# Performance work log

Measured on AMD Instinct MI355X. Metric: run time of the kernel, lower is better.

Reference implementation:

```python
import jax, jax.numpy as jnp
import numpy as np

B, N, F, H, OUT, K, L = 32, 2048, 3, 64, 128, 16, 3


def _edge_mlp(e, w1, b1, wo, bo):
    # Faithful to the given MLP.forward: layer1 -> ReLU -> output (layer2 is skipped!)
    return jax.nn.relu(e @ w1 + b1) @ wo + bo


def _dynamic_edge_conv(x, k, w1, b1, wo, bo):
    # x: [B, N, D]. kNN in feature space (self included, distance 0), per graph.
    sq = jnp.sum(x * x, axis=-1)                                   # [B, N]
    d2 = sq[:, :, None] + sq[:, None, :] - 2.0 * jnp.einsum('bnd,bmd->bnm', x, x)
    _, idx = jax.lax.top_k(-d2, k)                                 # [B, N, K]
    x_j = jax.vmap(lambda xb, ib: xb[ib])(x, idx)                  # [B, N, K, D] gather
    x_i = jnp.broadcast_to(x[:, :, None, :], x_j.shape)
    e = jnp.concatenate([x_i, x_j - x_i], axis=-1)                 # EdgeConv message [B,N,K,2D]
    h = _edge_mlp(e, w1, b1, wo, bo)                               # [B, N, K, H]
    return jnp.mean(h, axis=2)                                     # aggr='mean' -> [B, N, H]


def setup_inputs() -> dict:
    key = jax.random.key(0)
    ks = jax.random.split(key, 20)
    inp = {'x': jax.random.normal(ks[0], (B, N, F), dtype=jnp.float32)}
    kit = iter(ks[1:])
    for i in range(L):
        din = 2 * F if i == 0 else 2 * H
        inp[f'w1_{i}'] = jax.random.normal(next(kit), (din, H), jnp.float32) / np.sqrt(din)
        inp[f'b1_{i}'] = jnp.zeros((H,), jnp.float32)
        inp[f'wo_{i}'] = jax.random.normal(next(kit), (H, H), jnp.float32) / np.sqrt(H)
        inp[f'bo_{i}'] = jnp.zeros((H,), jnp.float32)
    inp['fw1'] = jax.random.normal(next(kit), (H, H), jnp.float32) / np.sqrt(H)
    inp['fb1'] = jnp.zeros((H,), jnp.float32)
    inp['fw2'] = jax.random.normal(next(kit), (H, OUT), jnp.float32) / np.sqrt(H)
    inp['fb2'] = jnp.zeros((OUT,), jnp.float32)
    return inp


def reference(x, w1_0, b1_0, wo_0, bo_0, w1_1, b1_1, wo_1, bo_1, w1_2, b1_2, wo_2, bo_2, fw1, fb1, fw2, fb2):
    layers = [(w1_0, b1_0, wo_0, bo_0), (w1_1, b1_1, wo_1, bo_1), (w1_2, b1_2, wo_2, bo_2)]
    h = x
    for (w1, b1, wo, bo) in layers:
        h = _dynamic_edge_conv(h, K, w1, b1, wo, bo)
    g = jnp.mean(h, axis=1)                                        # global_mean_pool -> [B, H]
    return jax.nn.relu(g @ fw1 + fb1) @ fw2 + fb2                  # [B, OUT]
```

## Files before the change

### kernel.cpp

```cpp
#include <hip/hip_runtime.h>

#define BB 32
#define NN 2048
#define FF 3
#define HH 64
#define OUTC 128
#define KK 16
#define BN (BB * NN)

typedef __attribute__((ext_vector_type(8))) __bf16 bf16x8;
typedef __attribute__((ext_vector_type(4))) float f32x4;

__device__ __forceinline__ unsigned int packkey(float d2, unsigned int m) {
    unsigned int bb = __builtin_bit_cast(unsigned int, d2);
    unsigned int msk = (unsigned int)((int)bb >> 31);
    unsigned int srt = bb ^ (msk | 0x80000000u);
    return (srt & 0xFFFFF800u) | m;
}

__device__ __forceinline__ void ce(unsigned int& a, unsigned int& b) {
    unsigned int lo = a < b ? a : b;
    unsigned int hi = a < b ? b : a;
    a = lo; b = hi;
}

__device__ __forceinline__ void sort16(unsigned int k[16]) {
#pragma unroll
    for (int p = 1; p < 16; p <<= 1)
#pragma unroll
        for (int q = p; q >= 1; q >>= 1)
#pragma unroll
            for (int j = q % p; j + q < 16; j += 2 * q)
#pragma unroll
                for (int i = 0; i < q; ++i) {
                    int x = i + j, y = i + j + q;
                    if (y < 16 && (x / (2 * p) == y / (2 * p))) ce(k[x], k[y]);
                }
}

__device__ __forceinline__ void merge16(unsigned int keys[16], const unsigned int nk[16]) {
    unsigned int t[16];
#pragma unroll
    for (int i = 0; i < 16; ++i) {
        unsigned int b = nk[15 - i];
        t[i] = keys[i] < b ? keys[i] : b;
    }
#pragma unroll
    for (int d = 8; d >= 1; d >>= 1)
#pragma unroll
        for (int i = 0; i < 16; ++i)
            if ((i & d) == 0) ce(t[i], t[i ^ d]);
#pragma unroll
    for (int i = 0; i < 16; ++i) keys[i] = t[i];
}

__global__ __launch_bounds__(256) void prep3_kernel(const float* __restrict__ x,
                                                    const float* __restrict__ w1,
                                                    const float* __restrict__ b1,
                                                    float* __restrict__ sqo,
                                                    float* __restrict__ P,
                                                    float* __restrict__ Q) {
    const int tid = threadIdx.x;
    const int h = tid & 63;
    const int pl = tid >> 6;
    const long p = (long)blockIdx.x * 4 + pl;
    const float* fp = x + p * 3;
    const float f0 = fp[0], f1 = fp[1], f2 = fp[2];
    if (h == 0) sqo[p] = f0 * f0 + f1 * f1 + f2 * f2;
    float accp = 0.f, accq = 0.f;
    const float fv[3] = {f0, f1, f2};
#pragma unroll
    for (int d = 0; d < 3; ++d) {
        float wa = w1[d * HH + h];
        float wb = w1[(3 + d) * HH + h];
        accp = fmaf(fv[d], wa - wb, accp);
        accq = fmaf(fv[d], wb, accq);
    }
    P[p * HH + h] = accp + b1[h];
    Q[p * HH + h] = accq;
}

__global__ __launch_bounds__(256) void prep64_kernel(const float* __restrict__ feat,
                                                     const float* __restrict__ w1,
                                                     const float* __restrict__ b1,
                                                     __bf16* __restrict__ fbf,
                                                     float* __restrict__ sqo,
                                                     float* __restrict__ P,
                                                     float* __restrict__ Q) {
    __shared__ float rows[64 * HH];
    const int tid = threadIdx.x;
    const int h = tid & 63;
    const int wv = tid >> 6;
    const long row0 = (long)blockIdx.x * 64;

    float wdiff[64], wbv[64];
#pragma unroll
    for (int d = 0; d < 64; ++d) {
        float wa = w1[d * HH + h];
        float wb_ = w1[(HH + d) * HH + h];
        wdiff[d] = wa - wb_;
        wbv[d] = wb_;
    }
    const float bv = b1[h];

    {
        const float4* src = (const float4*)(feat + row0 * HH);
        float4* dst = (float4*)rows;
#pragma unroll
        for (int i = 0; i < 4; ++i) dst[tid + 256 * i] = src[tid + 256 * i];
    }
    __syncthreads();

    for (int r = wv * 16; r < wv * 16 + 16; ++r) {
        const long p = row0 + r;
        float fvh = rows[r * HH + h];
        fbf[p * HH + h] = (__bf16)fvh;
        float s = fvh * fvh;
        s += __shfl_xor(s, 1);
        s += __shfl_xor(s, 2);
        s += __shfl_xor(s, 4);
        s += __shfl_xor(s, 8);
        s += __shfl_xor(s, 16);
        s += __shfl_xor(s, 32);
        if (h == 0) sqo[p] = s;

        float ap0 = 0.f, ap1 = 0.f, aq0 = 0.f, aq1 = 0.f;
#pragma unroll
        for (int d4 = 0; d4 < 16; ++d4) {
            float4 fv = *(const float4*)&rows[r * HH + d4 * 4];
            ap0 = fmaf(fv.x, wdiff[4 * d4 + 0], ap0);
            aq0 = fmaf(fv.x, wbv[4 * d4 + 0], aq0);
            ap1 = fmaf(fv.y, wdiff[4 * d4 + 1], ap1);
            aq1 = fmaf(fv.y, wbv[4 * d4 + 1], aq1);
            ap0 = fmaf(fv.z, wdiff[4 * d4 + 2], ap0);
            aq0 = fmaf(fv.z, wbv[4 * d4 + 2], aq0);
            ap1 = fmaf(fv.w, wdiff[4 * d4 + 3], ap1);
            aq1 = fmaf(fv.w, wbv[4 * d4 + 3], aq1);
        }
        P[p * HH + h] = (ap0 + ap1) + bv;
        Q[p * HH + h] = aq0 + aq1;
    }
}

__global__ __launch_bounds__(256) void knn3_filter_kernel(const float* __restrict__ x,
                                                          const float* __restrict__ sq,
                                                          unsigned short* __restrict__ idx32) {
    __shared__ float4 lds_c[256];
    __shared__ unsigned int Km[64 * 68];
    const int tid = threadIdx.x;
    const int xcd = blockIdx.x & 7;
    const int ii = blockIdx.x >> 3;
    const int b = xcd + 8 * (ii >> 5);
    const int rg = ii & 31;
    const long pbase = (long)b * NN;
    const int r = tid >> 2, slot = tid & 3;
    const int row = rg * 64 + r;

    const float* rp = x + (pbase + row) * 3;
    const float xr0 = rp[0], xr1 = rp[1], xr2 = rp[2];

    unsigned int keys[KK];
#pragma unroll
    for (int j = 0; j < KK; ++j) keys[j] = 0xFFFFFFFFu;

    float c0, c1, c2, c3;
    {
        const float* cp = x + (pbase + tid) * 3;
        c0 = cp[0]; c1 = cp[1]; c2 = cp[2]; c3 = sq[pbase + tid];
    }

    for (int t = 0; t < NN / 256; ++t) {
        __syncthreads();
        lds_c[tid] = make_float4(c0, c1, c2, c3);
        __syncthreads();
        if (t < NN / 256 - 1) {
            const int m = (t + 1) * 256 + tid;
            const float* cp = x + (pbase + m) * 3;
            c0 = cp[0]; c1 = cp[1]; c2 = cp[2]; c3 = sq[pbase + m];
        }
        const int cbase = slot * 64;
#pragma unroll
        for (int bb = 0; bb < 4; ++bb) {
            unsigned int nk[16];
#pragma unroll
            for (int cc = 0; cc < 16; ++cc) {
                float4 v = lds_c[cbase + bb * 16 + cc];
                float dot = fmaf(xr0, v.x, fmaf(xr1, v.y, xr2 * v.z));
                float d2 = fmaf(-2.0f, dot, v.w);
                nk[cc] = packkey(d2, (unsigned int)(t * 256 + cbase + bb * 16 + cc));
            }
            sort16(nk);
            merge16(keys, nk);
        }
    }

    {
        uint4* kw = (uint4*)&Km[r * 68 + slot * 16];
#pragma unroll
        for (int q = 0; q < 4; ++q)
            kw[q] = make_uint4(keys[4 * q], keys[4 * q + 1], keys[4 * q + 2], keys[4 * q + 3]);
    }
    __syncthreads();
    if (slot < 2) {
        const unsigned int* k0 = &Km[r * 68 + slot * 32];
        const unsigned int* k1 = k0 + 16;
        unsigned short ms[16];
#pragma unroll
        for (int j = 0; j < 16; ++j) {
            unsigned int a = k0[j], bv = k1[15 - j];
            ms[j] = (unsigned short)((a < bv ? a : bv) & 0x7FFu);
        }
        uint4* op = (uint4*)(idx32 + ((pbase + row) * 32 + slot * 16));
        op[0] = ((const uint4*)ms)[0];
        op[1] = ((const uint4*)ms)[1];
    }
}

#define APAD 80
#define DPAD 68

__global__ __launch_bounds__(256) void knn_filter_kernel(const __bf16* __restrict__ fbf,
                                                         const float* __restrict__ sq,
                                                         unsigned short* __restrict__ idx32) {
    __shared__ __align__(16) __bf16 Ab[64 * APAD];
    __shared__ __align__(16) __bf16 Bb[64 * APAD];
    __shared__ __align__(16) unsigned int Dt[64 * DPAD];
    __shared__ float SqC[64];

    const int tid = threadIdx.x;
    const int xcd = blockIdx.x & 7;
    const int ii = blockIdx.x >> 3;
    const int b = xcd + 8 * (ii >> 5);
    const int rg = ii & 31;
    const long pbase = (long)b * NN;
    const int row0 = rg * 64;
    const int ci = tid >> 2, ch = tid & 3;

    {
        const __bf16* src = fbf + (pbase + row0 + ci) * 64 + ch * 16;
        uint4 v0 = *(const uint4*)src;
        uint4 v1 = *(const uint4*)(src + 8);
        *(uint4*)&Ab[ci * APAD + ch * 16] = v0;
        *(uint4*)&Ab[ci * APAD + ch * 16 + 8] = v1;
    }
    __syncthreads();

    const int wv = tid >> 6, ln = tid & 63;
    const int n16 = ln & 15, quad = ln >> 4;
    bf16x8 af0, af1;
    {
        const __bf16* ap = &Ab[(wv * 16 + n16) * APAD + quad * 8];
        af0 = *(const bf16x8*)ap;
        af1 = *(const bf16x8*)(ap + 32);
    }

    const int r = tid >> 2, slot = tid & 3;
    unsigned int keys[KK];
#pragma unroll
    for (int j = 0; j < KK; ++j) keys[j] = 0xFFFFFFFFu;

    uint4 pv0, pv1;
    float psq;
    {
        const __bf16* src = fbf + (pbase + ci) * 64 + ch * 16;
        pv0 = *(const uint4*)src;
        pv1 = *(const uint4*)(src + 8);
        psq = (tid < 64) ? sq[pbase + tid] : 0.f;
    }

    for (int t = 0; t < NN / 64; ++t) {
        *(uint4*)&Bb[ci * APAD + ch * 16] = pv0;
        *(uint4*)&Bb[ci * APAD + ch * 16 + 8] = pv1;
        if (tid < 64) SqC[tid] = psq;
        __syncthreads();

#pragma unroll
        for (int ct = 0; ct < 4; ++ct) {
            const __bf16* bp = &Bb[(ct * 16 + n16) * APAD + quad * 8];
            bf16x8 bf0 = *(const bf16x8*)bp;
            bf16x8 bf1 = *(const bf16x8*)(bp + 32);
            f32x4 acc = {0.f, 0.f, 0.f, 0.f};
            acc = __builtin_amdgcn_mfma_f32_16x16x32_bf16(af0, bf0, acc, 0, 0, 0);
            acc = __builtin_amdgcn_mfma_f32_16x16x32_bf16(af1, bf1, acc, 0, 0, 0);
            const int ccol = ct * 16 + n16;
            const float sqc = SqC[ccol];
            const unsigned int m = (unsigned int)(t * 64 + ccol);
#pragma unroll
            for (int rr = 0; rr < 4; ++rr) {
                const int rrow = wv * 16 + quad * 4 + rr;
                Dt[rrow * DPAD + ccol] = packkey(fmaf(-2.0f, acc[rr], sqc), m);
            }
        }
        __syncthreads();

        if (t < NN / 64 - 1) {
            const __bf16* src = fbf + (pbase + (long)(t + 1) * 64 + ci) * 64 + ch * 16;
            pv0 = *(const uint4*)src;
            pv1 = *(const uint4*)(src + 8);
            if (tid < 64) psq = sq[pbase + (t + 1) * 64 + tid];
        }

        {
            const uint4* kp = (const uint4*)&Dt[r * DPAD + slot * 16];
            unsigned int nk[16];
#pragma unroll
            for (int q = 0; q < 4; ++q) {
                uint4 kv = kp[q];
                nk[4 * q + 0] = kv.x; nk[4 * q + 1] = kv.y;
                nk[4 * q + 2] = kv.z; nk[4 * q + 3] = kv.w;
            }
            sort16(nk);
            merge16(keys, nk);
        }
    }

    __syncthreads();
    {
        uint4* kw = (uint4*)&Dt[r * DPAD + slot * 16];
#pragma unroll
        for (int q = 0; q < 4; ++q)
            kw[q] = make_uint4(keys[4 * q], keys[4 * q + 1], keys[4 * q + 2], keys[4 * q + 3]);
    }
    __syncthreads();
    if (slot < 2) {
        const unsigned int* k0 = &Dt[r * DPAD + slot * 32];
        const unsigned int* k1 = k0 + 16;
        unsigned short ms[16];
#pragma unroll
        for (int j = 0; j < 16; ++j) {
            unsigned int a = k0[j], bv = k1[15 - j];
            ms[j] = (unsigned short)((a < bv ? a : bv) & 0x7FFu);
        }
        uint4* op = (uint4*)(idx32 + ((pbase + row0 + r) * 32 + slot * 16));
        op[0] = ((const uint4*)ms)[0];
        op[1] = ((const uint4*)ms)[1];
    }
}

template <int D>
__global__ __launch_bounds__(256) void rescore_gather_kernel(const float* __restrict__ feat,
                                                             const float* __restrict__ sq,
                                                             const unsigned short* __restrict__ idx32,
                                                             const float* __restrict__ P,
                                                             const float* __restrict__ Q,
                                                             const float* __restrict__ wo,
                                                             const float* __restrict__ bo,
                                                             float* __restrict__ outf) {
    __shared__ float rowf[8][D];
    __shared__ float Sc[8][32];
    __shared__ int Ji[8][32];
    __shared__ float Sq32[8][32];
    __shared__ int Li[8][KK];
    __shared__ float Rl[8][HH];
    const int tid = threadIdx.x;
    const int w = tid >> 6, ln = tid & 63;
    const int rw = ln >> 5, c = ln & 31;
    const int xcd = blockIdx.x & 7;
    const int ii = blockIdx.x >> 3;
    const int batch = xcd + 8 * (ii >> 8);
    const int rb = ii & 255;
    const long pbase = (long)batch * NN;
    const long pblk = pbase + (long)rb * 8;
    const long p = pblk + w * 2 + rw;
    const int row_ = w * 2 + rw;

    for (int i = tid; i < 8 * D; i += 256) rowf[i / D][i % D] = feat[pblk * D + i];
    {
        const int j0 = (int)idx32[p * 32 + c];
        Ji[row_][c] = j0;
        Sq32[row_][c] = sq[pbase + j0];
    }
    __syncthreads();

    if constexpr (D == 64) {
        const int cg = ln >> 2, e = ln & 3;
#pragma unroll
        for (int rr = 0; rr < 2; ++rr) {
#pragma unroll
            for (int pp = 0; pp < 2; ++pp) {
                const int row = w * 2 + rr;
                const int cand = pp * 16 + cg;
                const int jj = Ji[row][cand];
                const float* cb = feat + (pbase + jj) * 64;
                float part = 0.f;
#pragma unroll
                for (int blk = 0; blk < 4; ++blk) {
                    float4 cv = *(const float4*)(cb + blk * 16 + e * 4);
                    float4 rv = *(const float4*)&rowf[row][blk * 16 + e * 4];
                    part = fmaf(rv.x, cv.x, part);
                    part = fmaf(rv.y, cv.y, part);
                    part = fmaf(rv.z, cv.z, part);
                    part = fmaf(rv.w, cv.w, part);
                }
                part += __shfl_xor(part, 1);
                part += __shfl_xor(part, 2);
                if (e == 0) Sc[row][cand] = fmaf(-2.0f, part, Sq32[row][cand]);
            }
        }
    } else {
        const int jj = Ji[row_][c];
        const float* cp = feat + (pbase + jj) * 3;
        float dot = fmaf(rowf[row_][0], cp[0],
                    fmaf(rowf[row_][1], cp[1], rowf[row_][2] * cp[2]));
        Sc[row_][c] = fmaf(-2.0f, dot, Sq32[row_][c]);
    }
    __syncthreads();

    {
        const float score = Sc[row_][c];
        const int j = Ji[row_][c];
        int rank = 0;
#pragma unroll
        for (int m = 0; m < 32; ++m) {
            float dm = Sc[row_][m];
            int jm = Ji[row_][m];
            rank += (dm < score || (dm == score && jm < j)) ? 1 : 0;
        }
        if (rank < KK) Li[row_][rank] = j;
    }
    __syncthreads();

    const int h = tid & 63, pl = tid >> 6;
#pragma unroll
    for (int rr0 = 0; rr0 < 2; ++rr0) {
        const int rr = pl + rr0 * 4;
        const long pp = pblk + rr;
        const float Pv = P[pp * HH + h];
        float acc = 0.f;
#pragma unroll
        for (int k = 0; k < KK; ++k) {
            int j2 = Li[rr][k];
            acc += fmaxf(Pv + Q[(pbase + j2) * HH + h], 0.f);
        }
        Rl[rr][h] = acc * (1.f / KK);
    }
    __syncthreads();
#pragma unroll
    for (int rr0 = 0; rr0 < 2; ++rr0) {
        const int rr = pl + rr0 * 4;
        float o = bo[h];
#pragma unroll
        for (int l = 0; l < HH; ++l) o = fmaf(Rl[rr][l], wo[l * HH + h], o);
        outf[(pblk + rr) * HH + h] = o;
    }
}

__global__ __launch_bounds__(256) void pool_partial_kernel(const float* __restrict__ feat,
                                                           float* __restrict__ pp) {
    __shared__ float part[4][HH];
    const int batch = blockIdx.x >> 3;
    const int chk = blockIdx.x & 7;
    const int tid = threadIdx.x;
    const int h = tid & 63;
    const int sub = tid >> 6;
    float s = 0.f;
    const float* fp = feat + ((long)batch * NN + chk * 256 + sub * 64) * HH + h;
    for (int n = 0; n < 64; ++n) s += fp[(long)n * HH];
    part[sub][h] = s;
    __syncthreads();
    if (tid < HH)
        pp[(batch * 8 + chk) * HH + h] = part[0][h] + part[1][h] + part[2][h] + part[3][h];
}

__global__ __launch_bounds__(256) void head_kernel(const float* __restrict__ pp,
                                                   const float* __restrict__ fw1,
                                                   const float* __restrict__ fb1,
                                                   const float* __restrict__ fw2,
                                                   const float* __restrict__ fb2,
                                                   float* __restrict__ out) {
    __shared__ float g[HH];
    __shared__ float tl[HH];
    const int b = blockIdx.x;
    const int tid = threadIdx.x;
    if (tid < HH) {
        float s = 0.f;
#pragma unroll
        for (int c = 0; c < 8; ++c) s += pp[(b * 8 + c) * HH + tid];
        g[tid] = s * (1.f / NN);
    }
    __syncthreads();
    if (tid < HH) {
        float a = fb1[tid];
#pragma unroll
        for (int l = 0; l < HH; ++l) a = fmaf(g[l], fw1[l * HH + tid], a);
        tl[tid] = fmaxf(a, 0.f);
    }
    __syncthreads();
    if (tid < OUTC) {
        float o = fb2[tid];
#pragma unroll
        for (int l = 0; l < HH; ++l) o = fmaf(tl[l], fw2[l * OUTC + tid], o);
        out[(long)b * OUTC + tid] = o;
    }
}

extern "C" void kernel_launch(void* const* d_in, const int* in_sizes, int n_in,
                              void* d_out, int out_size, void* d_ws, size_t ws_size,
                              hipStream_t stream) {
    const float* x    = (const float*)d_in[0];
    const float* w1_0 = (const float*)d_in[1];
    const float* b1_0 = (const float*)d_in[2];
    const float* wo_0 = (const float*)d_in[3];
    const float* bo_0 = (const float*)d_in[4];
    const float* w1_1 = (const float*)d_in[5];
    const float* b1_1 = (const float*)d_in[6];
    const float* wo_1 = (const float*)d_in[7];
    const float* bo_1 = (const float*)d_in[8];
    const float* w1_2 = (const float*)d_in[9];
    const float* b1_2 = (const float*)d_in[10];
    const float* wo_2 = (const float*)d_in[11];
    const float* bo_2 = (const float*)d_in[12];
    const float* fw1  = (const float*)d_in[13];
    const float* fb1  = (const float*)d_in[14];
    const float* fw2  = (const float*)d_in[15];
    const float* fb2  = (const float*)d_in[16];
    float* out = (float*)d_out;

    float* featA = (float*)d_ws;
    float* featB = featA + (long)BN * HH;
    float* Pb    = featB + (long)BN * HH;
    float* Qb    = Pb + (long)BN * HH;
    float* sqb   = Qb + (long)BN * HH;
    unsigned short* idx32 = (unsigned short*)(sqb + BN);
    float* ppb   = (float*)(idx32 + (long)BN * 32);

    __bf16* fbf1 = (__bf16*)featB;
    __bf16* fbf2 = (__bf16*)featA;

    prep3_kernel<<<BN / 4, 256, 0, stream>>>(x, w1_0, b1_0, sqb, Pb, Qb);
    knn3_filter_kernel<<<BB * 32, 256, 0, stream>>>(x, sqb, idx32);
    rescore_gather_kernel<3><<<BN / 8, 256, 0, stream>>>(x, sqb, idx32, Pb, Qb, wo_0, bo_0, featA);

    prep64_kernel<<<BN / 64, 256, 0, stream>>>(featA, w1_1, b1_1, fbf1, sqb, Pb, Qb);
    knn_filter_kernel<<<BB * 32, 256, 0, stream>>>(fbf1, sqb, idx32);
    rescore_gather_kernel<64><<<BN / 8, 256, 0, stream>>>(featA, sqb, idx32, Pb, Qb, wo_1, bo_1, featB);

    prep64_kernel<<<BN / 64, 256, 0, stream>>>(featB, w1_2, b1_2, fbf2, sqb, Pb, Qb);
    knn_filter_kernel<<<BB * 32, 256, 0, stream>>>(fbf2, sqb, idx32);
    rescore_gather_kernel<64><<<BN / 8, 256, 0, stream>>>(featB, sqb, idx32, Pb, Qb, wo_2, bo_2, featA);

    pool_partial_kernel<<<BB * 8, 256, 0, stream>>>(featA, ppb);
    head_kernel<<<BB, 256, 0, stream>>>(ppb, fw1, fb1, fw2, fb2, out);
}
```

Before: 615.1 us.

## Swap MFMA operands to keep distances in registers and double-buffer candidate tiles

```diff
diff --git a/kernel.cpp b/kernel.cpp
--- a/kernel.cpp
+++ b/kernel.cpp
@@ -222,10 +222,8 @@
 __global__ __launch_bounds__(256) void knn_filter_kernel(const __bf16* __restrict__ fbf,
                                                          const float* __restrict__ sq,
                                                          unsigned short* __restrict__ idx32) {
-    __shared__ __align__(16) __bf16 Ab[64 * APAD];
-    __shared__ __align__(16) __bf16 Bb[64 * APAD];
-    __shared__ __align__(16) unsigned int Dt[64 * DPAD];
-    __shared__ float SqC[64];
+    __shared__ __align__(16) unsigned char smem[2 * 64 * APAD * 2];
+    __shared__ __align__(16) float SqD[2 * 64];
 
     const int tid = threadIdx.x;
     const int xcd = blockIdx.x & 7;
@@ -235,26 +233,16 @@
     const long pbase = (long)b * NN;
     const int row0 = rg * 64;
     const int ci = tid >> 2, ch = tid & 3;
-
-    {
-        const __bf16* src = fbf + (pbase + row0 + ci) * 64 + ch * 16;
-        uint4 v0 = *(const uint4*)src;
-        uint4 v1 = *(const uint4*)(src + 8);
-        *(uint4*)&Ab[ci * APAD + ch * 16] = v0;
-        *(uint4*)&Ab[ci * APAD + ch * 16 + 8] = v1;
-    }
-    __syncthreads();
-
     const int wv = tid >> 6, ln = tid & 63;
     const int n16 = ln & 15, quad = ln >> 4;
-    bf16x8 af0, af1;
-    {
-        const __bf16* ap = &Ab[(wv * 16 + n16) * APAD + quad * 8];
-        af0 = *(const bf16x8*)ap;
-        af1 = *(const bf16x8*)(ap + 32);
-    }
-
-    const int r = tid >> 2, slot = tid & 3;
+
+    bf16x8 rf0, rf1;
+    {
+        const __bf16* rp = fbf + (pbase + row0 + wv * 16 + n16) * 64 + quad * 8;
+        rf0 = *(const bf16x8*)rp;
+        rf1 = *(const bf16x8*)(rp + 32);
+    }
+
     unsigned int keys[KK];
 #pragma unroll
     for (int j = 0; j < KK; ++j) keys[j] = 0xFFFFFFFFu;
@@ -267,31 +255,18 @@
         pv1 = *(const uint4*)(src + 8);
         psq = (tid < 64) ? sq[pbase + tid] : 0.f;
     }
+    {
+        __bf16* B0 = (__bf16*)smem;
+        *(uint4*)&B0[ci * APAD + ch * 16] = pv0;
+        *(uint4*)&B0[ci * APAD + ch * 16 + 8] = pv1;
+        if (tid < 64) SqD[tid] = psq;
+    }
+    __syncthreads();
 
     for (int t = 0; t < NN / 64; ++t) {
-        *(uint4*)&Bb[ci * APAD + ch * 16] = pv0;
-        *(uint4*)&Bb[ci * APAD + ch * 16 + 8] = pv1;
-        if (tid < 64) SqC[tid] = psq;
-        __syncthreads();
-
-#pragma unroll
-        for (int ct = 0; ct < 4; ++ct) {
-            const __bf16* bp = &Bb[(ct * 16 + n16) * APAD + quad * 8];
-            bf16x8 bf0 = *(const bf16x8*)bp;
-            bf16x8 bf1 = *(const bf16x8*)(bp + 32);
-            f32x4 acc = {0.f, 0.f, 0.f, 0.f};
-            acc = __builtin_amdgcn_mfma_f32_16x16x32_bf16(af0, bf0, acc, 0, 0, 0);
-            acc = __builtin_amdgcn_mfma_f32_16x16x32_bf16(af1, bf1, acc, 0, 0, 0);
-            const int ccol = ct * 16 + n16;
-            const float sqc = SqC[ccol];
-            const unsigned int m = (unsigned int)(t * 64 + ccol);
-#pragma unroll
-            for (int rr = 0; rr < 4; ++rr) {
-                const int rrow = wv * 16 + quad * 4 + rr;
-                Dt[rrow * DPAD + ccol] = packkey(fmaf(-2.0f, acc[rr], sqc), m);
-            }
-        }
-        __syncthreads();
+        const int cur = t & 1;
+        const __bf16* Bc = (const __bf16*)smem + cur * 64 * APAD;
+        const float* Sc = SqD + cur * 64;
 
         if (t < NN / 64 - 1) {
             const __bf16* src = fbf + (pbase + (long)(t + 1) * 64 + ci) * 64 + ch * 16;
@@ -300,30 +275,46 @@
             if (tid < 64) psq = sq[pbase + (t + 1) * 64 + tid];
         }
 
-        {
-            const uint4* kp = (const uint4*)&Dt[r * DPAD + slot * 16];
-            unsigned int nk[16];
-#pragma unroll
-            for (int q = 0; q < 4; ++q) {
-                uint4 kv = kp[q];
-                nk[4 * q + 0] = kv.x; nk[4 * q + 1] = kv.y;
-                nk[4 * q + 2] = kv.z; nk[4 * q + 3] = kv.w;
-            }
-            sort16(nk);
-            merge16(keys, nk);
-        }
-    }
-
-    __syncthreads();
-    {
-        uint4* kw = (uint4*)&Dt[r * DPAD + slot * 16];
+        unsigned int nk[16];
+#pragma unroll
+        for (int ct = 0; ct < 4; ++ct) {
+            const __bf16* cp = &Bc[(ct * 16 + n16) * APAD + quad * 8];
+            bf16x8 cf0 = *(const bf16x8*)cp;
+            bf16x8 cf1 = *(const bf16x8*)(cp + 32);
+            f32x4 acc = {0.f, 0.f, 0.f, 0.f};
+            acc = __builtin_amdgcn_mfma_f32_16x16x32_bf16(cf0, rf0, acc, 0, 0, 0);
+            acc = __builtin_amdgcn_mfma_f32_16x16x32_bf16(cf1, rf1, acc, 0, 0, 0);
+            f32x4 sv = *(const f32x4*)&Sc[ct * 16 + quad * 4];
+            const unsigned int mb = (unsigned int)(t * 64 + ct * 16 + quad * 4);
+#pragma unroll
+            for (int rr = 0; rr < 4; ++rr)
+                nk[ct * 4 + rr] = packkey(fmaf(-2.0f, acc[rr], sv[rr]), mb + rr);
+        }
+
+        if (t < NN / 64 - 1) {
+            __bf16* Bn = (__bf16*)smem + (cur ^ 1) * 64 * APAD;
+            *(uint4*)&Bn[ci * APAD + ch * 16] = pv0;
+            *(uint4*)&Bn[ci * APAD + ch * 16 + 8] = pv1;
+            if (tid < 64) SqD[(cur ^ 1) * 64 + tid] = psq;
+        }
+
+        sort16(nk);
+        merge16(keys, nk);
+
+        __syncthreads();
+    }
+
+    unsigned int* stg = (unsigned int*)smem;
+    {
+        uint4* kw = (uint4*)&stg[(wv * 16 + n16) * DPAD + quad * 16];
 #pragma unroll
         for (int q = 0; q < 4; ++q)
             kw[q] = make_uint4(keys[4 * q], keys[4 * q + 1], keys[4 * q + 2], keys[4 * q + 3]);
     }
     __syncthreads();
+    const int r = tid >> 2, slot = tid & 3;
     if (slot < 2) {
-        const unsigned int* k0 = &Dt[r * DPAD + slot * 32];
+        const unsigned int* k0 = &stg[r * DPAD + slot * 32];
         const unsigned int* k1 = k0 + 16;
         unsigned short ms[16];
 #pragma unroll
```

Result: faster. 600.3 us (-2.4%).
